# Kernel tuning notes

Hardware: AMD Instinct MI355X
Metric: run time of the kernel (lower is better)

## Reference

```python
import jax, jax.numpy as jnp
import numpy as np

N, E, B, D, OUT_D = 10000, 160000, 64, 1024, 128

def setup_inputs() -> dict:
    key = jax.random.key(0)
    ks = jax.random.split(key, 18)
    s = 0.02
    return {
        "pro1_x": jax.random.normal(ks[0], (N, D), jnp.float32),
        "pro1_edge_index": jax.random.randint(ks[1], (2, E), 0, N, jnp.int64 if jax.config.jax_enable_x64 else jnp.int32),
        "pro1_batch": jnp.sort(jax.random.randint(ks[2], (N,), 0, B)),
        "pro2_x": jax.random.normal(ks[3], (N, D), jnp.float32),
        "pro2_edge_index": jax.random.randint(ks[4], (2, E), 0, N, jnp.int64 if jax.config.jax_enable_x64 else jnp.int32),
        "pro2_batch": jnp.sort(jax.random.randint(ks[5], (N,), 0, B)),
        "W1": jax.random.normal(ks[6], (D, D), jnp.float32) * s,
        "b1": jnp.zeros((D,), jnp.float32),
        "fc1_W": jax.random.normal(ks[7], (D, OUT_D), jnp.float32) * s,
        "fc1_b": jnp.zeros((OUT_D,), jnp.float32),
        "W2": jax.random.normal(ks[8], (D, D), jnp.float32) * s,
        "b2": jnp.zeros((D,), jnp.float32),
        "fc2_W": jax.random.normal(ks[9], (D, OUT_D), jnp.float32) * s,
        "fc2_b": jnp.zeros((OUT_D,), jnp.float32),
        "final_W": jax.random.normal(ks[10], (2 * OUT_D, 1), jnp.float32) * s,
        "final_b": jnp.zeros((1,), jnp.float32),
    }

def leaky_relu(x):
    return jnp.where(x >= 0, x, 0.01 * x)

def gcn_conv(x, edge_index, W, b):
    # PyG GCNConv with default add_self_loops + symmetric normalization
    src, dst = edge_index[0], edge_index[1]
    h = x @ W  # [N, D]
    deg = jnp.zeros((x.shape[0],), x.dtype).at[dst].add(1.0) + 1.0  # in-degree + self-loop
    dinv = jax.lax.rsqrt(deg)
    norm = dinv[src] * dinv[dst]  # [E]
    agg = jax.ops.segment_sum(h[src] * norm[:, None], dst, num_segments=x.shape[0])
    agg = agg + h * (1.0 / deg)[:, None]  # self-loop contribution: deg^-1/2 * deg^-1/2
    return agg + b

def global_mean_pool(x, batch, num_graphs):
    sums = jax.ops.segment_sum(x, batch, num_segments=num_graphs)
    cnt = jax.ops.segment_sum(jnp.ones((x.shape[0],), x.dtype), batch, num_segments=num_graphs)
    return sums / jnp.maximum(cnt, 1.0)[:, None]

def reference(pro1_x, pro1_edge_index, pro1_batch, pro2_x, pro2_edge_index, pro2_batch,
              W1, b1, fc1_W, fc1_b, W2, b2, fc2_W, fc2_b, final_W, final_b):
    # branch 1
    x = leaky_relu(gcn_conv(pro1_x, pro1_edge_index, W1, b1))
    x = global_mean_pool(x, pro1_batch, B)
    x = leaky_relu(x @ fc1_W + fc1_b)  # dropout is identity in eval
    # branch 2
    xt = leaky_relu(gcn_conv(pro2_x, pro2_edge_index, W2, b2))
    xt = global_mean_pool(xt, pro2_batch, B)
    xt = leaky_relu(xt @ fc2_W + fc2_b)
    combined = jnp.concatenate([x, xt], axis=1)  # [B, 256]
    return combined @ final_W + final_b
```

## Files before the change

kernel.cpp:

```cpp
#include <hip/hip_runtime.h>
#include <stdint.h>

typedef __attribute__((ext_vector_type(8))) short short8;
typedef __attribute__((ext_vector_type(8))) __bf16 bf16x8;
typedef __attribute__((ext_vector_type(4))) float f32x4;
typedef __attribute__((ext_vector_type(2))) float f32x2;

__device__ inline unsigned short f2bf(float f) {
  unsigned u = __float_as_uint(f);
  unsigned r = (u + 0x7FFFu + ((u >> 16) & 1u)) >> 16;
  return (unsigned short)r;
}
__device__ inline float bflo(unsigned v) { return __uint_as_float(v << 16); }
__device__ inline float bfhi(unsigned v) { return __uint_as_float(v & 0xFFFF0000u); }
__device__ inline bf16x8 as_bf(short8 v) { return __builtin_bit_cast(bf16x8, v); }
__device__ inline f32x2 up2(unsigned u) { f32x2 r; r.x = bflo(u); r.y = bfhi(u); return r; }
__device__ inline int lbound(const int* a, int n, int v) {
  int lo = 0, hi = n;
  while (lo < hi) { int m = (lo + hi) >> 1; if (a[m] < v) lo = m + 1; else hi = m; }
  return lo;
}

#define GLOAD_LDS16(gp, lp)                                                   \
  __builtin_amdgcn_global_load_lds(                                           \
      (const __attribute__((address_space(1))) void*)(gp),                    \
      (__attribute__((address_space(3))) void*)(lp), 16, 0, 0)

#define NG 1024
#define NSL 8

__global__ void prep1_kernel(const float* __restrict__ x0, const float* __restrict__ x1,
                             unsigned short* __restrict__ xb0, unsigned short* __restrict__ xb1,
                             const float* __restrict__ W0, const float* __restrict__ W1,
                             unsigned short* __restrict__ Wt0, unsigned short* __restrict__ Wt1,
                             const int* __restrict__ ei0, const int* __restrict__ ei1,
                             int* __restrict__ dg0, int* __restrict__ dg1,
                             int n, int mpad, int E, int CB) {
  __shared__ float tile[32][33];
  int br = blockIdx.y;
  int b = blockIdx.x;
  int t = threadIdx.x;
  if (b < CB) {
    const float* x = br ? x1 : x0;
    unsigned short* xb = br ? xb1 : xb0;
    long i = (long)b * 256 + t;
    long total = (long)mpad * 128;
    if (i >= total) return;
    long e0 = i * 8;
    int row = (int)(e0 >> 10);
    short8 v;
    if (row < n) {
      const float* s = x + e0;
      float4 fa = *(const float4*)(s);
      float4 fb = *(const float4*)(s + 4);
      v[0] = (short)f2bf(fa.x); v[1] = (short)f2bf(fa.y);
      v[2] = (short)f2bf(fa.z); v[3] = (short)f2bf(fa.w);
      v[4] = (short)f2bf(fb.x); v[5] = (short)f2bf(fb.y);
      v[6] = (short)f2bf(fb.z); v[7] = (short)f2bf(fb.w);
    } else {
      v = (short8)0;
    }
    *(short8*)(xb + e0) = v;
  } else if (b < CB + 1024) {
    const float* W = br ? W1 : W0;
    unsigned short* Wt = br ? Wt1 : Wt0;
    int bb = b - CB;
    int bx = bb & 31;
    int by = bb >> 5;
    int tx = t & 31, ty = t >> 5;
#pragma unroll
    for (int r = 0; r < 4; ++r) {
      int k = by * 32 + ty + r * 8;
      tile[ty + r * 8][tx] = W[(long)k * 1024 + bx * 32 + tx];
    }
    __syncthreads();
#pragma unroll
    for (int r = 0; r < 4; ++r) {
      int nrow = bx * 32 + ty + r * 8;
      int kcol = by * 32 + tx;
      Wt[(long)nrow * 1024 + kcol] = f2bf(tile[tx][ty + r * 8]);
    }
  } else {
    const int* ei = br ? ei1 : ei0;
    int* degi = br ? dg1 : dg0;
    int e = (b - CB - 1024) * 256 + t;
    if (e >= E) return;
    atomicAdd(&degi[ei[E + e]], 1);
  }
}

__global__ __launch_bounds__(1024) void scan2_kernel(
    const int* __restrict__ degA, int* __restrict__ offA, int* __restrict__ curA,
    const int* __restrict__ degB, int* __restrict__ offB, int* __restrict__ curB, int n) {
  const int* deg = blockIdx.x ? degB : degA;
  int* off = blockIdx.x ? offB : offA;
  int* cur = blockIdx.x ? curB : curA;
  __shared__ int wsum[17];
  int t = threadIdx.x, lane = t & 63, w = t >> 6;
  int CH = (n + 1023) >> 10;
  int i0 = t * CH;
  int s = 0;
  for (int i = 0; i < CH; ++i) {
    int idx = i0 + i;
    s += (idx < n) ? ((deg[idx] + 4) & ~3) : 0;
  }
  int inc = s;
  for (int d = 1; d < 64; d <<= 1) {
    int x = __shfl_up(inc, d);
    if (lane >= d) inc += x;
  }
  if (lane == 63) wsum[w] = inc;
  __syncthreads();
  if (t == 0) {
    int r = 0;
    for (int k = 0; k < 16; ++k) { int x = wsum[k]; wsum[k] = r; r += x; }
    wsum[16] = r;
  }
  __syncthreads();
  int run = wsum[w] + inc - s;
  for (int i = 0; i < CH; ++i) {
    int idx = i0 + i;
    if (idx < n) {
      off[idx] = run;
      cur[idx] = run;
      run += (deg[idx] + 4) & ~3;
    }
  }
  if (t == 0) off[n] = wsum[16];
}

__global__ void prep2_kernel(const int* __restrict__ ei0, const int* __restrict__ ei1,
                             const int* __restrict__ dg0, const int* __restrict__ dg1,
                             int* __restrict__ cur0, int* __restrict__ cur1,
                             uint2* __restrict__ cw0, uint2* __restrict__ cw1,
                             const int* __restrict__ off0, const int* __restrict__ off1,
                             int* __restrict__ rng0, int* __restrict__ rng1,
                             int E, int N, int FB) {
  int br = blockIdx.y;
  int b = blockIdx.x;
  int t = threadIdx.x;
  if (b < FB) {
    const int* ei = br ? ei1 : ei0;
    const int* dg = br ? dg1 : dg0;
    int* cur = br ? cur1 : cur0;
    uint2* cw = br ? cw1 : cw0;
    int e = b * 256 + t;
    if (e >= E + N) return;
    int s, d; float w;
    if (e < E) {
      s = ei[e]; d = ei[E + e];
      w = rsqrtf((float)(dg[s] + 1)) * rsqrtf((float)(dg[d] + 1));
    } else {
      s = e - E; d = s;
      w = 1.0f / (float)(dg[s] + 1);
    }
    int p = atomicAdd(&cur[d], 1);
    uint2 v; v.x = (unsigned)s * 2048u; v.y = __float_as_uint(w);
    cw[p] = v;
  } else {
    const int* off = br ? off1 : off0;
    int* rng = br ? rng1 : rng0;
    int q = (b - FB) * 256 + t;
    if (q > NG) return;
    if (q == NG) { rng[q] = N; return; }
    long Etot = off[N];
    long target = (long)q * Etot;
    int lo = 0, hi = N;
    while (lo < hi) {
      int mid = (lo + hi) >> 1;
      if ((long)off[mid] * NG >= target) hi = mid; else lo = mid + 1;
    }
    rng[q] = lo;
  }
}

#define BM 128
#define BN 128
#define BK 64

__global__ __launch_bounds__(256) void gemm_bf16_kernel(
    const unsigned short* __restrict__ A0, const unsigned short* __restrict__ A1,
    const unsigned short* __restrict__ B0, const unsigned short* __restrict__ B1,
    unsigned short* __restrict__ C0, unsigned short* __restrict__ C1,
    int Nn, int K) {
  const unsigned short* A = blockIdx.z ? A1 : A0;
  const unsigned short* Bt = blockIdx.z ? B1 : B0;
  unsigned short* C = blockIdx.z ? C1 : C0;
  __shared__ alignas(16) unsigned short As[BM * BK];
  __shared__ alignas(16) unsigned short Bs[BN * BK];
  int x = blockIdx.x;
  long m0 = (long)((x >> 6) * 8 + (x & 7)) * BM;
  long n0 = (long)((x >> 3) & 7) * BN;
  int t = threadIdx.x;
  int lane = t & 63;
  int w = t >> 6;
  int wm = (w >> 1) * 64, wn = (w & 1) * 64;
  int l3 = lane >> 3;
  int gsw = (lane & 7) ^ l3;
  int srowb = w * 8 + l3;
  const unsigned short* Ag = A + (m0 + srowb) * K + gsw * 8;
  const unsigned short* Bg = Bt + (n0 + srowb) * K + gsw * 8;
  unsigned short* AsP = As + t * 8;
  unsigned short* BsP = Bs + t * 8;
  int fr = lane & 15;
  int c0 = (lane >> 4) ^ (lane & 7);
  const unsigned short* afp0 = As + (wm + fr) * BK + c0 * 8;
  const unsigned short* afp1 = As + (wm + fr) * BK + (c0 ^ 4) * 8;
  const unsigned short* bfp0 = Bs + (wn + fr) * BK + c0 * 8;
  const unsigned short* bfp1 = Bs + (wn + fr) * BK + (c0 ^ 4) * 8;
  f32x4 acc[4][4] = {};
  for (int k0 = 0; k0 < K; k0 += BK) {
    __syncthreads();
#pragma unroll
    for (int j = 0; j < 4; ++j) {
      GLOAD_LDS16(Ag + (long)(j * 32) * K + k0, AsP + j * 2048);
      GLOAD_LDS16(Bg + (long)(j * 32) * K + k0, BsP + j * 2048);
    }
    __syncthreads();
    short8 af[4][2], bf[4][2];
#pragma unroll
    for (int i = 0; i < 4; ++i) {
      af[i][0] = *(const short8*)(afp0 + i * 16 * BK);
      af[i][1] = *(const short8*)(afp1 + i * 16 * BK);
    }
#pragma unroll
    for (int i = 0; i < 4; ++i) {
      bf[i][0] = *(const short8*)(bfp0 + i * 16 * BK);
      bf[i][1] = *(const short8*)(bfp1 + i * 16 * BK);
    }
#pragma unroll
    for (int i = 0; i < 4; ++i)
#pragma unroll
      for (int j = 0; j < 4; ++j) {
        acc[i][j] = __builtin_amdgcn_mfma_f32_16x16x32_bf16(as_bf(af[i][0]), as_bf(bf[j][0]),
                                                            acc[i][j], 0, 0, 0);
        acc[i][j] = __builtin_amdgcn_mfma_f32_16x16x32_bf16(as_bf(af[i][1]), as_bf(bf[j][1]),
                                                            acc[i][j], 0, 0, 0);
      }
  }
  int cr = (lane >> 4) * 4;
  int cc = lane & 15;
#pragma unroll
  for (int i = 0; i < 4; ++i)
#pragma unroll
    for (int j = 0; j < 4; ++j) {
      long row = m0 + wm + i * 16 + cr;
      long col = n0 + wn + j * 16 + cc;
      unsigned short* cp = C + row * Nn + col;
#pragma unroll
      for (int r = 0; r < 4; ++r)
        cp[(long)r * Nn] = f2bf(acc[i][j][r]);
    }
}

__global__ __launch_bounds__(256) void agg_pool_kernel(
    const unsigned short* __restrict__ H0, const unsigned short* __restrict__ H1,
    const int* __restrict__ off0, const int* __restrict__ off1,
    const uint2* __restrict__ cw0, const uint2* __restrict__ cw1,
    const int* __restrict__ b0, const int* __restrict__ b1,
    const int* __restrict__ rng0, const int* __restrict__ rng1,
    const float* __restrict__ bias0, const float* __restrict__ bias1,
    float* __restrict__ pool0, float* __restrict__ pool1,
    float* __restrict__ scr0, float* __restrict__ scr1,
    int* __restrict__ gid0, int* __restrict__ gid1) {
  int br = blockIdx.y;
  const uint8_t* Hb = (const uint8_t*)(br ? H1 : H0);
  const int* off = br ? off1 : off0;
  const uint2* cw = br ? cw1 : cw0;
  const int* batch = br ? b1 : b0;
  const int* rng = br ? rng1 : rng0;
  const float* bias = br ? bias1 : bias0;
  float* pool = br ? pool1 : pool0;
  float* scratch = br ? scr1 : scr0;
  int* gid = br ? gid1 : gid0;

  int t = threadIdx.x;
  int wv = t >> 6, lane = t & 63, qw = lane >> 4, l16 = lane & 15;
  int slice = blockIdx.x & 7;
  int part = blockIdx.x >> 3;
  int q = part * 4 + wv;
  int d0 = slice * 128 + l16 * 8;
  unsigned d0b = (unsigned)d0 * 2;
  float4 bv0 = *(const float4*)(bias + d0);
  float4 bv1 = *(const float4*)(bias + d0 + 4);
  int na = rng[q], nb = rng[q + 1];
  int g0 = -1, g1 = -1;
  if (na < nb) {
    float bv[8] = {bv0.x, bv0.y, bv0.z, bv0.w, bv1.x, bv1.y, bv1.z, bv1.w};
    float pacc[8] = {};
    f32x2 a2[4] = {};
    int curg = batch[na];
    int fi = 0;
    int nd = na;
    int ee = off[na + 1];
    int eend = off[nb];
    int e = off[na];
    uint2 cc = cw[e + qw];
    uint2 cn = cw[e + 4 + qw];
    uint4 hc = *(const uint4*)(Hb + (cc.x + d0b));
#pragma unroll 2
    for (; e < eend; e += 4) {
      uint4 hn = *(const uint4*)(Hb + (cn.x + d0b));
      uint2 c2 = cw[e + 8 + qw];
      float w = __uint_as_float(cc.y);
      f32x2 w2; w2.x = w; w2.y = w;
      a2[0] += w2 * up2(hc.x);
      a2[1] += w2 * up2(hc.y);
      a2[2] += w2 * up2(hc.z);
      a2[3] += w2 * up2(hc.w);
      cc = cn; cn = c2; hc = hn;
      if (e + 4 == ee) {
#pragma unroll
        for (int k = 0; k < 8; ++k) {
          float v = (k & 1) ? a2[k >> 1].y : a2[k >> 1].x;
          v += __shfl_xor(v, 16);
          v += __shfl_xor(v, 32);
          v += bv[k];
          pacc[k] += (v >= 0.f) ? v : 0.01f * v;
        }
#pragma unroll
        for (int k = 0; k < 4; ++k) { a2[k].x = 0.f; a2[k].y = 0.f; }
        ++nd;
        if (nd < nb) {
          ee = off[nd + 1];
          int g = batch[nd];
          if (g != curg) {
            if (fi == 0) {
              g0 = curg;
              if (qw == 0) {
                float* sp = scratch + ((long)q * 2 + 0) * 1024 + d0;
                *(float4*)sp = make_float4(pacc[0], pacc[1], pacc[2], pacc[3]);
                *(float4*)(sp + 4) = make_float4(pacc[4], pacc[5], pacc[6], pacc[7]);
              }
            } else {
              if (qw == 0) {
                float* pp = pool + (long)curg * 1024 + d0;
#pragma unroll
                for (int k = 0; k < 8; ++k) atomicAdd(pp + k, pacc[k]);
              }
            }
            ++fi;
#pragma unroll
            for (int k = 0; k < 8; ++k) pacc[k] = 0.f;
            curg = g;
          }
        }
      }
    }
    if (fi == 0) {
      g0 = curg;
      if (qw == 0) {
        float* sp = scratch + ((long)q * 2 + 0) * 1024 + d0;
        *(float4*)sp = make_float4(pacc[0], pacc[1], pacc[2], pacc[3]);
        *(float4*)(sp + 4) = make_float4(pacc[4], pacc[5], pacc[6], pacc[7]);
      }
    } else {
      g1 = curg;
      if (qw == 0) {
        float* sp = scratch + ((long)q * 2 + 1) * 1024 + d0;
        *(float4*)sp = make_float4(pacc[0], pacc[1], pacc[2], pacc[3]);
        *(float4*)(sp + 4) = make_float4(pacc[4], pacc[5], pacc[6], pacc[7]);
      }
    }
  }
  if (slice == 0 && lane == 0) {
    gid[q * 2] = g0;
    gid[q * 2 + 1] = g1;
  }
}

__global__ __launch_bounds__(256) void fc_final_kernel(
    const float* __restrict__ pool1, const float* __restrict__ pool2,
    const float* __restrict__ scr0, const float* __restrict__ scr1,
    const int* __restrict__ gid0, const int* __restrict__ gid1,
    const int* __restrict__ rng0, const int* __restrict__ rng1,
    const int* __restrict__ b0, const int* __restrict__ b1, int N,
    const float* __restrict__ fc1W, const float* __restrict__ fc1b,
    const float* __restrict__ fc2W, const float* __restrict__ fc2b,
    const float* __restrict__ finW, const float* __restrict__ finb,
    float* __restrict__ out) {
  __shared__ float p1[1024], p2[1024];
  __shared__ float red[256];
  int g = blockIdx.x, t = threadIdx.x;
  int gs0 = lbound(b0, N, g), ge0 = lbound(b0, N, g + 1);
  float ic1 = 1.0f / (float)max(ge0 - gs0, 1);
  int qlo0 = max(lbound(rng0, NG + 1, gs0 + 1) - 1, 0);
  int qhi0 = min(lbound(rng0, NG + 1, ge0) - 1, NG - 1);
  int gs1 = lbound(b1, N, g), ge1 = lbound(b1, N, g + 1);
  float ic2 = 1.0f / (float)max(ge1 - gs1, 1);
  int qlo1 = max(lbound(rng1, NG + 1, gs1 + 1) - 1, 0);
  int qhi1 = min(lbound(rng1, NG + 1, ge1) - 1, NG - 1);
  for (int i = t; i < 1024; i += 256) {
    float s1 = pool1[(long)g * 1024 + i];
    for (int q = qlo0; q <= qhi0; ++q) {
      if (gid0[q * 2] == g)     s1 += scr0[((long)q * 2 + 0) * 1024 + i];
      if (gid0[q * 2 + 1] == g) s1 += scr0[((long)q * 2 + 1) * 1024 + i];
    }
    p1[i] = s1 * ic1;
    float s2 = pool2[(long)g * 1024 + i];
    for (int q = qlo1; q <= qhi1; ++q) {
      if (gid1[q * 2] == g)     s2 += scr1[((long)q * 2 + 0) * 1024 + i];
      if (gid1[q * 2 + 1] == g) s2 += scr1[((long)q * 2 + 1) * 1024 + i];
    }
    p2[i] = s2 * ic2;
  }
  __syncthreads();
  float contrib;
  if (t < 128) {
    float a = 0.f;
    for (int k = 0; k < 1024; ++k) a += p1[k] * fc1W[(long)k * 128 + t];
    a += fc1b[t];
    a = a >= 0.f ? a : 0.01f * a;
    contrib = a * finW[t];
  } else {
    int j = t - 128;
    float a = 0.f;
    for (int k = 0; k < 1024; ++k) a += p2[k] * fc2W[(long)k * 128 + j];
    a += fc2b[j];
    a = a >= 0.f ? a : 0.01f * a;
    contrib = a * finW[128 + j];
  }
  red[t] = contrib;
  __syncthreads();
  for (int s = 128; s; s >>= 1) {
    if (t < s) red[t] += red[t + s];
    __syncthreads();
  }
  if (t == 0) out[g] = red[0] + finb[0];
}

extern "C" void kernel_launch(void* const* d_in, const int* in_sizes, int n_in,
                              void* d_out, int out_size, void* d_ws, size_t ws_size,
                              hipStream_t stream) {
  (void)n_in; (void)ws_size;
  const float* xs[2]   = {(const float*)d_in[0], (const float*)d_in[3]};
  const int* eis[2]    = {(const int*)d_in[1], (const int*)d_in[4]};
  const int* bts[2]    = {(const int*)d_in[2], (const int*)d_in[5]};
  const float* Ws[2]   = {(const float*)d_in[6], (const float*)d_in[10]};
  const float* bs[2]   = {(const float*)d_in[7], (const float*)d_in[11]};
  const float* fc1W = (const float*)d_in[8];
  const float* fc1b = (const float*)d_in[9];
  const float* fc2W = (const float*)d_in[12];
  const float* fc2b = (const float*)d_in[13];
  const float* finW = (const float*)d_in[14];
  const float* finb = (const float*)d_in[15];
  float* out = (float*)d_out;

  const int N = in_sizes[2];
  const int E = in_sizes[1] / 2;
  const int Mpad = ((N + 1023) / 1024) * 1024;
  const int MT = Mpad / BM;
  const int CWCAP = E + 4 * N + 64;

  uint8_t* ws = (uint8_t*)d_ws;
  size_t o = 0;
  auto alloc = [&](size_t bytes) { size_t r = o; o += (bytes + 255) & ~(size_t)255; return r; };
  size_t degi_o[2] = {alloc((size_t)N * 4), alloc((size_t)N * 4)};
  size_t pool_o[2] = {alloc((size_t)out_size * 1024 * 4), alloc((size_t)out_size * 1024 * 4)};
  size_t cw_o[2]   = {alloc((size_t)CWCAP * 8), alloc((size_t)CWCAP * 8)};
  size_t zero_end = o;
  size_t cur_o[2]  = {alloc((size_t)N * 4), alloc((size_t)N * 4)};
  size_t off_o[2]  = {alloc((size_t)(N + 1) * 4), alloc((size_t)(N + 1) * 4)};
  size_t rng_o[2]  = {alloc((size_t)(NG + 1) * 4), alloc((size_t)(NG + 1) * 4)};
  size_t gid_o[2]  = {alloc((size_t)NG * 2 * 4), alloc((size_t)NG * 2 * 4)};
  size_t scr_o[2]  = {alloc((size_t)NG * 2 * 1024 * 4), alloc((size_t)NG * 2 * 1024 * 4)};
  size_t xb_o[2]   = {alloc((size_t)Mpad * 1024 * 2), alloc((size_t)Mpad * 1024 * 2)};
  size_t wt_o[2]   = {alloc((size_t)1024 * 1024 * 2), alloc((size_t)1024 * 1024 * 2)};
  size_t h_o[2]    = {alloc((size_t)Mpad * 1024 * 2), alloc((size_t)Mpad * 1024 * 2)};

  (void)hipMemsetAsync(ws, 0, zero_end, stream);

  const int CB = (int)(((long)Mpad * 128 + 255) / 256);
  const int DB = (E + 255) / 256;
  prep1_kernel<<<dim3(CB + 1024 + DB, 2), 256, 0, stream>>>(
      xs[0], xs[1], (unsigned short*)(ws + xb_o[0]), (unsigned short*)(ws + xb_o[1]),
      Ws[0], Ws[1], (unsigned short*)(ws + wt_o[0]), (unsigned short*)(ws + wt_o[1]),
      eis[0], eis[1], (int*)(ws + degi_o[0]), (int*)(ws + degi_o[1]),
      N, Mpad, E, CB);
  scan2_kernel<<<2, 1024, 0, stream>>>(
      (const int*)(ws + degi_o[0]), (int*)(ws + off_o[0]), (int*)(ws + cur_o[0]),
      (const int*)(ws + degi_o[1]), (int*)(ws + off_o[1]), (int*)(ws + cur_o[1]), N);
  const int FB = (E + N + 255) / 256;
  const int RB = (NG + 256) / 256;
  prep2_kernel<<<dim3(FB + RB, 2), 256, 0, stream>>>(
      eis[0], eis[1], (const int*)(ws + degi_o[0]), (const int*)(ws + degi_o[1]),
      (int*)(ws + cur_o[0]), (int*)(ws + cur_o[1]),
      (uint2*)(ws + cw_o[0]), (uint2*)(ws + cw_o[1]),
      (const int*)(ws + off_o[0]), (const int*)(ws + off_o[1]),
      (int*)(ws + rng_o[0]), (int*)(ws + rng_o[1]), E, N, FB);
  gemm_bf16_kernel<<<dim3(MT * 8, 1, 2), 256, 0, stream>>>(
      (const unsigned short*)(ws + xb_o[0]), (const unsigned short*)(ws + xb_o[1]),
      (const unsigned short*)(ws + wt_o[0]), (const unsigned short*)(ws + wt_o[1]),
      (unsigned short*)(ws + h_o[0]), (unsigned short*)(ws + h_o[1]), 1024, 1024);
  agg_pool_kernel<<<dim3((NG / 4) * NSL, 2), 256, 0, stream>>>(
      (const unsigned short*)(ws + h_o[0]), (const unsigned short*)(ws + h_o[1]),
      (const int*)(ws + off_o[0]), (const int*)(ws + off_o[1]),
      (const uint2*)(ws + cw_o[0]), (const uint2*)(ws + cw_o[1]),
      bts[0], bts[1],
      (const int*)(ws + rng_o[0]), (const int*)(ws + rng_o[1]),
      bs[0], bs[1],
      (float*)(ws + pool_o[0]), (float*)(ws + pool_o[1]),
      (float*)(ws + scr_o[0]), (float*)(ws + scr_o[1]),
      (int*)(ws + gid_o[0]), (int*)(ws + gid_o[1]));
  fc_final_kernel<<<out_size, 256, 0, stream>>>(
      (const float*)(ws + pool_o[0]), (const float*)(ws + pool_o[1]),
      (const float*)(ws + scr_o[0]), (const float*)(ws + scr_o[1]),
      (const int*)(ws + gid_o[0]), (const int*)(ws + gid_o[1]),
      (const int*)(ws + rng_o[0]), (const int*)(ws + rng_o[1]),
      bts[0], bts[1], N,
      fc1W, fc1b, fc2W, fc2b, finW, finb, out);
}
```

Baseline: 257.3 us.

## Split pooled-mean reduction and FC head into two wider-parallel kernels

```diff
diff --git a/kernel.cpp b/kernel.cpp
--- a/kernel.cpp
+++ b/kernel.cpp
@@ -369,64 +369,74 @@
   }
 }
 
-__global__ __launch_bounds__(256) void fc_final_kernel(
-    const float* __restrict__ pool1, const float* __restrict__ pool2,
+__global__ __launch_bounds__(256) void pool_reduce_kernel(
     const float* __restrict__ scr0, const float* __restrict__ scr1,
     const int* __restrict__ gid0, const int* __restrict__ gid1,
+    const int* __restrict__ b0, const int* __restrict__ b1,
     const int* __restrict__ rng0, const int* __restrict__ rng1,
-    const int* __restrict__ b0, const int* __restrict__ b1, int N,
+    const float* __restrict__ pool0, const float* __restrict__ pool1,
+    float* __restrict__ pm0, float* __restrict__ pm1,
+    const float* __restrict__ finb, float* __restrict__ out, int N, int nb_) {
+  int br = blockIdx.y;
+  const float* scratch = br ? scr1 : scr0;
+  const int* gid = br ? gid1 : gid0;
+  const int* batch = br ? b1 : b0;
+  const int* rng = br ? rng1 : rng0;
+  const float* pool = br ? pool1 : pool0;
+  float* pm = br ? pm1 : pm0;
+  int g = blockIdx.x >> 2;
+  int slice = blockIdx.x & 3;
+  int tid = threadIdx.x;
+  if (br == 0 && blockIdx.x == 0 && tid < nb_) out[tid] = finb[0];
+  int gs = lbound(batch, N, g), ge = lbound(batch, N, g + 1);
+  float ic = 1.0f / (float)max(ge - gs, 1);
+  int qlo = max(lbound(rng, NG + 1, gs + 1) - 1, 0);
+  int qhi = min(lbound(rng, NG + 1, ge) - 1, NG - 1);
+  long idx = (long)g * 1024 + slice * 256 + tid;
+  float s = pool[idx];
+  if (gs < ge) {
+    for (int q = qlo; q <= qhi; ++q) {
+      int a = gid[q * 2], b = gid[q * 2 + 1];
+      if (a == g) s += scratch[((long)q * 2 + 0) * 1024 + slice * 256 + tid];
+      if (b == g) s += scratch[((long)q * 2 + 1) * 1024 + slice * 256 + tid];
+    }
+  }
+  pm[idx] = s * ic;
+}
+
+__global__ __launch_bounds__(512) void fc_head_kernel(
+    const float* __restrict__ pm0, const float* __restrict__ pm1,
     const float* __restrict__ fc1W, const float* __restrict__ fc1b,
     const float* __restrict__ fc2W, const float* __restrict__ fc2b,
-    const float* __restrict__ finW, const float* __restrict__ finb,
-    float* __restrict__ out) {
-  __shared__ float p1[1024], p2[1024];
-  __shared__ float red[256];
-  int g = blockIdx.x, t = threadIdx.x;
-  int gs0 = lbound(b0, N, g), ge0 = lbound(b0, N, g + 1);
-  float ic1 = 1.0f / (float)max(ge0 - gs0, 1);
-  int qlo0 = max(lbound(rng0, NG + 1, gs0 + 1) - 1, 0);
-  int qhi0 = min(lbound(rng0, NG + 1, ge0) - 1, NG - 1);
-  int gs1 = lbound(b1, N, g), ge1 = lbound(b1, N, g + 1);
-  float ic2 = 1.0f / (float)max(ge1 - gs1, 1);
-  int qlo1 = max(lbound(rng1, NG + 1, gs1 + 1) - 1, 0);
-  int qhi1 = min(lbound(rng1, NG + 1, ge1) - 1, NG - 1);
-  for (int i = t; i < 1024; i += 256) {
-    float s1 = pool1[(long)g * 1024 + i];
-    for (int q = qlo0; q <= qhi0; ++q) {
-      if (gid0[q * 2] == g)     s1 += scr0[((long)q * 2 + 0) * 1024 + i];
-      if (gid0[q * 2 + 1] == g) s1 += scr0[((long)q * 2 + 1) * 1024 + i];
-    }
-    p1[i] = s1 * ic1;
-    float s2 = pool2[(long)g * 1024 + i];
-    for (int q = qlo1; q <= qhi1; ++q) {
-      if (gid1[q * 2] == g)     s2 += scr1[((long)q * 2 + 0) * 1024 + i];
-      if (gid1[q * 2 + 1] == g) s2 += scr1[((long)q * 2 + 1) * 1024 + i];
-    }
-    p2[i] = s2 * ic2;
-  }
+    const float* __restrict__ finW, float* __restrict__ out) {
+  __shared__ float p[1024];
+  __shared__ float red[512];
+  int g = blockIdx.x, br = blockIdx.y, t = threadIdx.x;
+  const float* pm = br ? pm1 : pm0;
+  const float* W = br ? fc2W : fc1W;
+  const float* bb = br ? fc2b : fc1b;
+  for (int i = t; i < 1024; i += 512) p[i] = pm[(long)g * 1024 + i];
   __syncthreads();
-  float contrib;
+  int col = t & 127, kq = t >> 7;
+  const float* Wp = W + (long)(kq * 256) * 128 + col;
+  const float* pk = p + kq * 256;
+  float a = 0.f;
+#pragma unroll 8
+  for (int k = 0; k < 256; ++k) a += pk[k] * Wp[(long)k * 128];
+  red[t] = a;
+  __syncthreads();
   if (t < 128) {
-    float a = 0.f;
-    for (int k = 0; k < 1024; ++k) a += p1[k] * fc1W[(long)k * 128 + t];
-    a += fc1b[t];
-    a = a >= 0.f ? a : 0.01f * a;
-    contrib = a * finW[t];
-  } else {
-    int j = t - 128;
-    float a = 0.f;
-    for (int k = 0; k < 1024; ++k) a += p2[k] * fc2W[(long)k * 128 + j];
-    a += fc2b[j];
-    a = a >= 0.f ? a : 0.01f * a;
-    contrib = a * finW[128 + j];
-  }
-  red[t] = contrib;
+    float s = red[t] + red[t + 128] + red[t + 256] + red[t + 384];
+    s += bb[t];
+    s = s >= 0.f ? s : 0.01f * s;
+    red[t] = s * finW[br * 128 + t];
+  }
   __syncthreads();
-  for (int s = 128; s; s >>= 1) {
-    if (t < s) red[t] += red[t + s];
+  for (int st = 64; st; st >>= 1) {
+    if (t < st) red[t] += red[t + st];
     __syncthreads();
   }
-  if (t == 0) out[g] = red[0] + finb[0];
+  if (t == 0) atomicAdd(&out[g], red[0]);
 }
 
 extern "C" void kernel_launch(void* const* d_in, const int* in_sizes, int n_in,
@@ -464,6 +474,7 @@
   size_t rng_o[2]  = {alloc((size_t)(NG + 1) * 4), alloc((size_t)(NG + 1) * 4)};
   size_t gid_o[2]  = {alloc((size_t)NG * 2 * 4), alloc((size_t)NG * 2 * 4)};
   size_t scr_o[2]  = {alloc((size_t)NG * 2 * 1024 * 4), alloc((size_t)NG * 2 * 1024 * 4)};
+  size_t pm_o[2]   = {alloc((size_t)out_size * 1024 * 4), alloc((size_t)out_size * 1024 * 4)};
   size_t xb_o[2]   = {alloc((size_t)Mpad * 1024 * 2), alloc((size_t)Mpad * 1024 * 2)};
   size_t wt_o[2]   = {alloc((size_t)1024 * 1024 * 2), alloc((size_t)1024 * 1024 * 2)};
   size_t h_o[2]    = {alloc((size_t)Mpad * 1024 * 2), alloc((size_t)Mpad * 1024 * 2)};
@@ -502,11 +513,15 @@
       (float*)(ws + pool_o[0]), (float*)(ws + pool_o[1]),
       (float*)(ws + scr_o[0]), (float*)(ws + scr_o[1]),
       (int*)(ws + gid_o[0]), (int*)(ws + gid_o[1]));
-  fc_final_kernel<<<out_size, 256, 0, stream>>>(
-      (const float*)(ws + pool_o[0]), (const float*)(ws + pool_o[1]),
+  pool_reduce_kernel<<<dim3(out_size * 4, 2), 256, 0, stream>>>(
       (const float*)(ws + scr_o[0]), (const float*)(ws + scr_o[1]),
       (const int*)(ws + gid_o[0]), (const int*)(ws + gid_o[1]),
+      bts[0], bts[1],
       (const int*)(ws + rng_o[0]), (const int*)(ws + rng_o[1]),
-      bts[0], bts[1], N,
-      fc1W, fc1b, fc2W, fc2b, finW, finb, out);
-}
+      (const float*)(ws + pool_o[0]), (const float*)(ws + pool_o[1]),
+      (float*)(ws + pm_o[0]), (float*)(ws + pm_o[1]),
+      finb, out, N, out_size);
+  fc_head_kernel<<<dim3(out_size, 2), 512, 0, stream>>>(
+      (const float*)(ws + pm_o[0]), (const float*)(ws + pm_o[1]),
+      fc1W, fc1b, fc2W, fc2b, finW, out);
+}
```

Measured after the change: 210.3 us (median of 2 runs). 1.22x faster.
